# Performance work log

Hardware: AMD Instinct MI355X
Metric: run time of the kernel (lower is better)

## Reference

```python
import jax, jax.numpy as jnp
import numpy as np

B, S, E, H = 2, 2048, 768, 12
DK = E // H


def setup_inputs() -> dict:
    key = jax.random.key(0)
    ks = jax.random.split(key, 8)
    scale = 1.0 / np.sqrt(E)
    return {
        "key": jax.random.normal(ks[0], (B, S, E), jnp.float32),
        "query": jax.random.normal(ks[1], (B, S, E), jnp.float32),
        "value": jax.random.normal(ks[2], (B, S, E), jnp.float32),
        "mask": jax.random.randint(ks[3], (1, 1, S, S), 0, 2, jnp.int32),
        # nn.Linear params (w_k used for q/k/v as in the source; w_o output proj)
        "Wk": jax.random.uniform(ks[4], (E, E), jnp.float32, -scale, scale),
        "bk": jax.random.uniform(ks[5], (E,), jnp.float32, -scale, scale),
        "Wo": jax.random.uniform(ks[6], (E, E), jnp.float32, -scale, scale),
        "bo": jax.random.uniform(ks[7], (E,), jnp.float32, -scale, scale),
    }


def reference(key, query, value, mask, Wk, bk, Wo, bo):
    # NOTE: source module (faithfully) projects q, k, v all with w_k.
    k = (key @ Wk.T + bk).reshape(B, S, H, DK).transpose(0, 2, 1, 3)    # [B,H,S,DK]
    q = (query @ Wk.T + bk).reshape(B, S, H, DK).transpose(0, 2, 1, 3)
    v = (value @ Wk.T + bk).reshape(B, S, H, DK).transpose(0, 2, 1, 3)
    # quirk: scores MULTIPLIED by sqrt(d_k) (source bug, preserved)
    scores = jnp.einsum("bhsd,bhtd->bhst", q, k) * jnp.sqrt(jnp.float32(DK))
    # quirk: masked positions set to 1e-6 (not -inf), BEFORE softmax
    scores = jnp.where(mask == 0, jnp.float32(1e-6), scores)
    # dropout=0.0 -> identity (applied pre-softmax in source)
    attn = jax.nn.softmax(scores, axis=-1)                               # [B,H,S,S]
    x = jnp.einsum("bhst,bhtd->bhsd", attn, v)                           # [B,H,S,DK]
    x = x.transpose(0, 2, 1, 3).reshape(B, S, E)
    return x @ Wo.T + bo
```

## Files before the change

### kernel.cpp

```cpp
#include <hip/hip_runtime.h>

#define BB 2
#define SS 2048
#define EE 768
#define HH 12
#define DKK 64

typedef _Float16 h16;
typedef _Float16 half8 __attribute__((ext_vector_type(8)));
typedef _Float16 h16x4 __attribute__((ext_vector_type(4)));
typedef float f32x4 __attribute__((ext_vector_type(4)));

__global__ void pack_mask_k(const int* __restrict__ mask, unsigned* __restrict__ mp) {
    int idx = blockIdx.x * 256 + threadIdx.x;
    int base = idx * 32;
    const int4* m4 = (const int4*)(mask + base);
    unsigned w = 0;
#pragma unroll
    for (int i = 0; i < 8; ++i) {
        int4 v = m4[i];
        if (v.x) w |= 1u << (i * 4 + 0);
        if (v.y) w |= 1u << (i * 4 + 1);
        if (v.z) w |= 1u << (i * 4 + 2);
        if (v.w) w |= 1u << (i * 4 + 3);
    }
    mp[idx] = w;
}

__launch_bounds__(256)
__global__ void proj_gemm_k(const float* __restrict__ srcK, const float* __restrict__ srcQ,
                            const float* __restrict__ srcV, const float* __restrict__ Wk,
                            const float* __restrict__ bk,
                            h16* __restrict__ kh, h16* __restrict__ qh, h16* __restrict__ vtp) {
    __shared__ h16 As[128 * 64];
    __shared__ h16 Bs[128 * 64];
    const int bid = blockIdx.x;
    const int idx = (bid & 7) * 72 + (bid >> 3);
    const int z = idx / 192;
    const int rem = idx % 192;
    const int n0 = (rem % 6) * 128, m0 = (rem / 6) * 128;
    const float* src = (z == 0) ? srcK : ((z == 1) ? srcQ : srcV);
    const int tid = threadIdx.x, lane = tid & 63, wid = tid >> 6;
    const int wr = wid >> 1, wc = wid & 1;
    f32x4 acc[4][4] = {};

    for (int k0 = 0; k0 < EE; k0 += 64) {
#pragma unroll
        for (int it = 0; it < 4; ++it) {
            int e8 = it * 256 + tid;
            int row = e8 >> 3, g = e8 & 7;
            const float* pa = src + (m0 + row) * EE + k0 + g * 8;
            const float* pb = Wk + (n0 + row) * EE + k0 + g * 8;
            float4 a0 = *(const float4*)pa, a1 = *(const float4*)(pa + 4);
            float4 b0 = *(const float4*)pb, b1 = *(const float4*)(pb + 4);
            half8 ha = {(h16)a0.x, (h16)a0.y, (h16)a0.z, (h16)a0.w,
                        (h16)a1.x, (h16)a1.y, (h16)a1.z, (h16)a1.w};
            half8 hb = {(h16)b0.x, (h16)b0.y, (h16)b0.z, (h16)b0.w,
                        (h16)b1.x, (h16)b1.y, (h16)b1.z, (h16)b1.w};
            int sw = (g ^ (row & 7)) << 4;
            *(half8*)((char*)As + row * 128 + sw) = ha;
            *(half8*)((char*)Bs + row * 128 + sw) = hb;
        }
        __syncthreads();
#pragma unroll
        for (int ks = 0; ks < 2; ++ks) {
            half8 a[4], b[4];
#pragma unroll
            for (int rf = 0; rf < 4; ++rf) {
                int row = wr * 64 + rf * 16 + (lane & 15);
                int g = (ks * 4 + (lane >> 4)) ^ (row & 7);
                a[rf] = *(const half8*)((const char*)As + row * 128 + (g << 4));
            }
#pragma unroll
            for (int cf = 0; cf < 4; ++cf) {
                int row = wc * 64 + cf * 16 + (lane & 15);
                int g = (ks * 4 + (lane >> 4)) ^ (row & 7);
                b[cf] = *(const half8*)((const char*)Bs + row * 128 + (g << 4));
            }
#pragma unroll
            for (int rf = 0; rf < 4; ++rf)
#pragma unroll
                for (int cf = 0; cf < 4; ++cf)
                    acc[rf][cf] = __builtin_amdgcn_mfma_f32_16x16x32_f16(a[rf], b[cf], acc[rf][cf], 0, 0, 0);
        }
        __syncthreads();
    }
    if (z == 2) {
#pragma unroll
        for (int rf = 0; rf < 4; ++rf)
#pragma unroll
            for (int cf = 0; cf < 4; ++cf) {
                int n = n0 + wc * 64 + cf * 16 + (lane & 15);
                float bias = bk[n];
                int h = n >> 6, d = n & 63;
                int mb = m0 + wr * 64 + rf * 16 + (lane >> 4) * 4;
                int b = mb >> 11, s = mb & 2047;
                h16x4 pv = {(h16)(acc[rf][cf][0] + bias), (h16)(acc[rf][cf][1] + bias),
                            (h16)(acc[rf][cf][2] + bias), (h16)(acc[rf][cf][3] + bias)};
                *(h16x4*)(vtp + ((long)((b * HH + h) * 64 + d)) * SS + s) = pv;
            }
    } else {
        h16* dst = (z == 0) ? kh : qh;
#pragma unroll
        for (int rf = 0; rf < 4; ++rf)
#pragma unroll
            for (int cf = 0; cf < 4; ++cf) {
                int n = n0 + wc * 64 + cf * 16 + (lane & 15);
                float bias = bk[n];
                int h = n >> 6, d = n & 63;
#pragma unroll
                for (int j = 0; j < 4; ++j) {
                    int m = m0 + wr * 64 + rf * 16 + (lane >> 4) * 4 + j;
                    int b = m >> 11, s = m & 2047;
                    dst[(((long)(b * HH + h) * SS + s) << 6) + d] = (h16)(acc[rf][cf][j] + bias);
                }
            }
    }
}

struct StageRegs { half8 k[2], v[2]; };

__device__ __forceinline__ void ld_stage(StageRegs& r, const h16* __restrict__ kg,
                                         const h16* __restrict__ vg,
                                         int kv0, int wid, int lane) {
    int rr = lane >> 3;
    int sg = (lane & 7) ^ rr;
#pragma unroll
    for (int i = 0; i < 2; ++i) {
        int row = wid * 16 + i * 8 + rr;
        r.k[i] = *(const half8*)(kg + (long)(kv0 + row) * DKK + sg * 8);
        r.v[i] = *(const half8*)(vg + (long)row * SS + kv0 + sg * 8);
    }
}

__device__ __forceinline__ void st_stage(h16* __restrict__ kl, h16* __restrict__ vl,
                                         const StageRegs& r, int wid, int lane) {
#pragma unroll
    for (int i = 0; i < 2; ++i) {
        *(half8*)(kl + wid * 1024 + i * 512 + lane * 8) = r.k[i];
        *(half8*)(vl + wid * 1024 + i * 512 + lane * 8) = r.v[i];
    }
}

__launch_bounds__(256, 3)
__global__ void attn_k(const h16* __restrict__ qh, const h16* __restrict__ kh,
                       const h16* __restrict__ vt, const unsigned long long* __restrict__ mp,
                       h16* __restrict__ xh) {
    __shared__ h16 Kbuf[2][4096];
    __shared__ h16 Vbuf[2][4096];
    __shared__ char Ps[8192];
    const int tid = threadIdx.x;
    const int lane = tid & 63, wid = tid >> 6;
    const int l = lane & 15, g = lane >> 4;
    const int bid = blockIdx.x;
    const int idx = (bid & 7) * 96 + (bid >> 3);
    const int q0 = (idx & 31) * 64 + wid * 16;
    const int bh = idx >> 5;
    const long base = (long)bh * SS * DKK;
    const h16* kg = kh + base;
    const h16* vg = vt + base;
    char* pbase = Ps + wid * 2048;

    half8 qf0, qf1;
    {
        const h16* qp = qh + base + (long)(q0 + l) * DKK + g * 8;
        qf0 = *(const half8*)qp;
        qf1 = *(const half8*)(qp + 32);
    }
    const unsigned long long* mrow = mp + (long)(q0 + l) * (SS / 64);

    f32x4 o[4] = {};
    float m2 = -INFINITY, lsum = 0.f;
    const float K2 = 8.0f * 1.44269504f;
    const float C2 = 1e-6f * 1.44269504f;

    StageRegs sr;
    ld_stage(sr, kg, vg, 0, wid, lane);
    st_stage(Kbuf[0], Vbuf[0], sr, wid, lane);
    __syncthreads();

    for (int t = 0; t < 32; ++t) {
        const h16* Kl = Kbuf[t & 1];
        const h16* Vl = Vbuf[t & 1];
        ld_stage(sr, kg, vg, ((t + 1) & 31) * 64, wid, lane);
        half8 ka[4], kb[4];
#pragma unroll
        for (int cf = 0; cf < 4; ++cf) {
            int row = cf * 16 + l;
            const h16* kp = Kl + row * 64;
            ka[cf] = *(const half8*)(kp + ((g ^ (row & 7)) << 3));
            kb[cf] = *(const half8*)(kp + (((4 + g) ^ (row & 7)) << 3));
        }
        f32x4 s[4];
        __builtin_amdgcn_s_setprio(1);
#pragma unroll
        for (int cf = 0; cf < 4; ++cf) {
            f32x4 z = {};
            z = __builtin_amdgcn_mfma_f32_16x16x32_f16(ka[cf], qf0, z, 0, 0, 0);
            z = __builtin_amdgcn_mfma_f32_16x16x32_f16(kb[cf], qf1, z, 0, 0, 0);
            s[cf] = z;
        }
        __builtin_amdgcn_s_setprio(0);
        unsigned long long mw = mrow[t];
        unsigned w0 = (unsigned)mw, w1 = (unsigned)(mw >> 32);
#pragma unroll
        for (int cf = 0; cf < 4; ++cf) {
            unsigned wcb = (cf & 2) ? w1 : w0;
#pragma unroll
            for (int j = 0; j < 4; ++j) {
                unsigned sh = ((cf & 1) << 4) + g * 4 + j;
                s[cf][j] = ((wcb >> sh) & 1u) ? s[cf][j] * K2 : C2;
            }
        }
        float pmax = fmaxf(fmaxf(s[0][0], s[0][1]), fmaxf(s[0][2], s[0][3]));
#pragma unroll
        for (int cf = 1; cf < 4; ++cf)
            pmax = fmaxf(pmax, fmaxf(fmaxf(s[cf][0], s[cf][1]), fmaxf(s[cf][2], s[cf][3])));
        if (!__all(pmax <= m2 + 11.0f)) {
            pmax = fmaxf(pmax, __shfl_xor(pmax, 16));
            pmax = fmaxf(pmax, __shfl_xor(pmax, 32));
            float mnew = fmaxf(m2, pmax);
            float alpha = __builtin_amdgcn_exp2f(m2 - mnew);
#pragma unroll
            for (int df = 0; df < 4; ++df)
#pragma unroll
                for (int j = 0; j < 4; ++j) o[df][j] *= alpha;
            lsum *= alpha;
            m2 = mnew;
        }
        float rs = 0.f;
#pragma unroll
        for (int cf = 0; cf < 4; ++cf)
#pragma unroll
            for (int j = 0; j < 4; ++j) {
                float p = __builtin_amdgcn_exp2f(s[cf][j] - m2);
                s[cf][j] = p;
                rs += p;
            }
        lsum += rs;
#pragma unroll
        for (int cf = 0; cf < 4; ++cf) {
            h16x4 pk = {(h16)s[cf][0], (h16)s[cf][1], (h16)s[cf][2], (h16)s[cf][3]};
            int gran = (2 * cf + (g >> 1)) ^ (l & 7);
            *(h16x4*)(pbase + l * 128 + gran * 16 + (g & 1) * 8) = pk;
        }
#pragma unroll
        for (int ks = 0; ks < 2; ++ks) {
            int gr = (ks * 4 + g) ^ (l & 7);
            half8 pf = *(const half8*)(pbase + l * 128 + gr * 16);
            half8 vk[4];
#pragma unroll
            for (int df = 0; df < 4; ++df) {
                int row = df * 16 + l;
                vk[df] = *(const half8*)(Vl + row * 64 + (((ks * 4 + g) ^ (row & 7)) << 3));
            }
            __builtin_amdgcn_s_setprio(1);
#pragma unroll
            for (int df = 0; df < 4; ++df)
                o[df] = __builtin_amdgcn_mfma_f32_16x16x32_f16(vk[df], pf, o[df], 0, 0, 0);
            __builtin_amdgcn_s_setprio(0);
        }
        st_stage(Kbuf[(t + 1) & 1], Vbuf[(t + 1) & 1], sr, wid, lane);
        __syncthreads();
    }

    lsum += __shfl_xor(lsum, 16);
    lsum += __shfl_xor(lsum, 32);
    float inv = 1.0f / lsum;
    int b = bh / HH, h = bh % HH;
    h16* xp = xh + (long)(b * SS + q0 + l) * EE + h * 64 + g * 4;
#pragma unroll
    for (int df = 0; df < 4; ++df) {
        h16x4 v4 = {(h16)(o[df][0] * inv), (h16)(o[df][1] * inv),
                    (h16)(o[df][2] * inv), (h16)(o[df][3] * inv)};
        *(h16x4*)(xp + df * 16) = v4;
    }
}

__launch_bounds__(256)
__global__ void out_gemm_k(const h16* __restrict__ xh, const float* __restrict__ Wo,
                           const float* __restrict__ bo, float* __restrict__ out) {
    __shared__ h16 As[128 * 64];
    __shared__ h16 Bs[128 * 64];
    const int bid = blockIdx.x;
    const int idx = (bid & 7) * 24 + (bid >> 3);
    const int n0 = (idx % 6) * 128, m0 = (idx / 6) * 128;
    const int tid = threadIdx.x, lane = tid & 63, wid = tid >> 6;
    const int wr = wid >> 1, wc = wid & 1;
    f32x4 acc[4][4] = {};

    for (int k0 = 0; k0 < EE; k0 += 64) {
#pragma unroll
        for (int it = 0; it < 4; ++it) {
            int e8 = it * 256 + tid;
            int row = e8 >> 3, g = e8 & 7;
            half8 ha = *(const half8*)(xh + (m0 + row) * EE + k0 + g * 8);
            const float* pb = Wo + (n0 + row) * EE + k0 + g * 8;
            float4 b0 = *(const float4*)pb, b1 = *(const float4*)(pb + 4);
            half8 hb = {(h16)b0.x, (h16)b0.y, (h16)b0.z, (h16)b0.w,
                        (h16)b1.x, (h16)b1.y, (h16)b1.z, (h16)b1.w};
            int sw = (g ^ (row & 7)) << 4;
            *(half8*)((char*)As + row * 128 + sw) = ha;
            *(half8*)((char*)Bs + row * 128 + sw) = hb;
        }
        __syncthreads();
#pragma unroll
        for (int ks = 0; ks < 2; ++ks) {
            half8 a[4], b[4];
#pragma unroll
            for (int rf = 0; rf < 4; ++rf) {
                int row = wr * 64 + rf * 16 + (lane & 15);
                int g = (ks * 4 + (lane >> 4)) ^ (row & 7);
                a[rf] = *(const half8*)((const char*)As + row * 128 + (g << 4));
            }
#pragma unroll
            for (int cf = 0; cf < 4; ++cf) {
                int row = wc * 64 + cf * 16 + (lane & 15);
                int g = (ks * 4 + (lane >> 4)) ^ (row & 7);
                b[cf] = *(const half8*)((const char*)Bs + row * 128 + (g << 4));
            }
#pragma unroll
            for (int rf = 0; rf < 4; ++rf)
#pragma unroll
                for (int cf = 0; cf < 4; ++cf)
                    acc[rf][cf] = __builtin_amdgcn_mfma_f32_16x16x32_f16(a[rf], b[cf], acc[rf][cf], 0, 0, 0);
        }
        __syncthreads();
    }
#pragma unroll
    for (int rf = 0; rf < 4; ++rf)
#pragma unroll
        for (int cf = 0; cf < 4; ++cf) {
            int n = n0 + wc * 64 + cf * 16 + (lane & 15);
            float bias = bo[n];
#pragma unroll
            for (int j = 0; j < 4; ++j) {
                int m = m0 + wr * 64 + rf * 16 + (lane >> 4) * 4 + j;
                out[(long)m * EE + n] = acc[rf][cf][j] + bias;
            }
        }
}

extern "C" void kernel_launch(void* const* d_in, const int* in_sizes, int n_in,
                              void* d_out, int out_size, void* d_ws, size_t ws_size,
                              hipStream_t stream) {
    const float* key   = (const float*)d_in[0];
    const float* query = (const float*)d_in[1];
    const float* value = (const float*)d_in[2];
    const int*   mask  = (const int*)d_in[3];
    const float* Wk    = (const float*)d_in[4];
    const float* bk    = (const float*)d_in[5];
    const float* Wo    = (const float*)d_in[6];
    const float* bo    = (const float*)d_in[7];

    char* ws = (char*)d_ws;
    h16* qh = (h16*)(ws + 0);
    h16* kh = (h16*)(ws + 6291456);
    h16* vt = (h16*)(ws + 12582912);
    h16* xh = (h16*)(ws + 18874368);
    unsigned* mp = (unsigned*)(ws + 25165824);
    float* out = (float*)d_out;

    hipLaunchKernelGGL(pack_mask_k, dim3(SS * SS / 32 / 256), dim3(256), 0, stream, mask, mp);
    hipLaunchKernelGGL(proj_gemm_k, dim3(576), dim3(256), 0, stream,
                       key, query, value, Wk, bk, kh, qh, vt);
    hipLaunchKernelGGL(attn_k, dim3(SS / 64 * BB * HH), dim3(256), 0, stream,
                       qh, kh, vt, (const unsigned long long*)mp, xh);
    hipLaunchKernelGGL(out_gemm_k, dim3(192), dim3(256), 0, stream, xh, Wo, bo, out);
}
```

Baseline: 132.0 us.

## Prefetch next K-tile into registers in projection and output GEMMs

Both the QKV projection GEMM and the output GEMM now load the next 64-wide K-slice from global memory into registers before running the MFMAs on the current shared-memory tile. The prefetched data is converted and written to LDS after the compute, so global load latency overlaps with matrix math. MFMA sections are also wrapped in s_setprio to raise wave priority. This adds register pressure from the staged float4 buffers, which could reduce occupancy.

```diff
diff --git a/kernel.cpp b/kernel.cpp
--- a/kernel.cpp
+++ b/kernel.cpp
@@ -44,24 +44,39 @@
     const int wr = wid >> 1, wc = wid & 1;
     f32x4 acc[4][4] = {};
 
+    float4 ra[4][2], rb[4][2];
+#define PROJ_ISSUE(k0)                                                        \
+    _Pragma("unroll")                                                         \
+    for (int it = 0; it < 4; ++it) {                                          \
+        int e8 = it * 256 + tid;                                              \
+        int row = e8 >> 3, g = e8 & 7;                                        \
+        const float* pa = src + (m0 + row) * EE + (k0) + g * 8;               \
+        const float* pb = Wk + (n0 + row) * EE + (k0) + g * 8;                \
+        ra[it][0] = *(const float4*)pa; ra[it][1] = *(const float4*)(pa + 4); \
+        rb[it][0] = *(const float4*)pb; rb[it][1] = *(const float4*)(pb + 4); \
+    }
+#define PROJ_WRITE()                                                          \
+    _Pragma("unroll")                                                         \
+    for (int it = 0; it < 4; ++it) {                                          \
+        int e8 = it * 256 + tid;                                              \
+        int row = e8 >> 3, g = e8 & 7;                                        \
+        half8 ha = {(h16)ra[it][0].x, (h16)ra[it][0].y, (h16)ra[it][0].z,     \
+                    (h16)ra[it][0].w, (h16)ra[it][1].x, (h16)ra[it][1].y,     \
+                    (h16)ra[it][1].z, (h16)ra[it][1].w};                      \
+        half8 hb = {(h16)rb[it][0].x, (h16)rb[it][0].y, (h16)rb[it][0].z,     \
+                    (h16)rb[it][0].w, (h16)rb[it][1].x, (h16)rb[it][1].y,     \
+                    (h16)rb[it][1].z, (h16)rb[it][1].w};                      \
+        int sw = (g ^ (row & 7)) << 4;                                        \
+        *(half8*)((char*)As + row * 128 + sw) = ha;                           \
+        *(half8*)((char*)Bs + row * 128 + sw) = hb;                           \
+    }
+
+    PROJ_ISSUE(0)
+    PROJ_WRITE()
+    __syncthreads();
+
     for (int k0 = 0; k0 < EE; k0 += 64) {
-#pragma unroll
-        for (int it = 0; it < 4; ++it) {
-            int e8 = it * 256 + tid;
-            int row = e8 >> 3, g = e8 & 7;
-            const float* pa = src + (m0 + row) * EE + k0 + g * 8;
-            const float* pb = Wk + (n0 + row) * EE + k0 + g * 8;
-            float4 a0 = *(const float4*)pa, a1 = *(const float4*)(pa + 4);
-            float4 b0 = *(const float4*)pb, b1 = *(const float4*)(pb + 4);
-            half8 ha = {(h16)a0.x, (h16)a0.y, (h16)a0.z, (h16)a0.w,
-                        (h16)a1.x, (h16)a1.y, (h16)a1.z, (h16)a1.w};
-            half8 hb = {(h16)b0.x, (h16)b0.y, (h16)b0.z, (h16)b0.w,
-                        (h16)b1.x, (h16)b1.y, (h16)b1.z, (h16)b1.w};
-            int sw = (g ^ (row & 7)) << 4;
-            *(half8*)((char*)As + row * 128 + sw) = ha;
-            *(half8*)((char*)Bs + row * 128 + sw) = hb;
-        }
-        __syncthreads();
+        if (k0 + 64 < EE) { PROJ_ISSUE(k0 + 64) }
 #pragma unroll
         for (int ks = 0; ks < 2; ++ks) {
             half8 a[4], b[4];
@@ -77,14 +92,22 @@
                 int g = (ks * 4 + (lane >> 4)) ^ (row & 7);
                 b[cf] = *(const half8*)((const char*)Bs + row * 128 + (g << 4));
             }
+            __builtin_amdgcn_s_setprio(1);
 #pragma unroll
             for (int rf = 0; rf < 4; ++rf)
 #pragma unroll
                 for (int cf = 0; cf < 4; ++cf)
                     acc[rf][cf] = __builtin_amdgcn_mfma_f32_16x16x32_f16(a[rf], b[cf], acc[rf][cf], 0, 0, 0);
+            __builtin_amdgcn_s_setprio(0);
         }
         __syncthreads();
-    }
+        if (k0 + 64 < EE) {
+            PROJ_WRITE()
+            __syncthreads();
+        }
+    }
+#undef PROJ_ISSUE
+#undef PROJ_WRITE
     if (z == 2) {
 #pragma unroll
         for (int rf = 0; rf < 4; ++rf)
@@ -289,21 +312,36 @@
     const int wr = wid >> 1, wc = wid & 1;
     f32x4 acc[4][4] = {};
 
+    half8 ra[4];
+    float4 rb[4][2];
+#define OG_ISSUE(k0)                                                          \
+    _Pragma("unroll")                                                         \
+    for (int it = 0; it < 4; ++it) {                                          \
+        int e8 = it * 256 + tid;                                              \
+        int row = e8 >> 3, g = e8 & 7;                                        \
+        ra[it] = *(const half8*)(xh + (m0 + row) * EE + (k0) + g * 8);        \
+        const float* pb = Wo + (n0 + row) * EE + (k0) + g * 8;                \
+        rb[it][0] = *(const float4*)pb; rb[it][1] = *(const float4*)(pb + 4); \
+    }
+#define OG_WRITE()                                                            \
+    _Pragma("unroll")                                                         \
+    for (int it = 0; it < 4; ++it) {                                          \
+        int e8 = it * 256 + tid;                                              \
+        int row = e8 >> 3, g = e8 & 7;                                        \
+        half8 hb = {(h16)rb[it][0].x, (h16)rb[it][0].y, (h16)rb[it][0].z,     \
+                    (h16)rb[it][0].w, (h16)rb[it][1].x, (h16)rb[it][1].y,     \
+                    (h16)rb[it][1].z, (h16)rb[it][1].w};                      \
+        int sw = (g ^ (row & 7)) << 4;                                        \
+        *(half8*)((char*)As + row * 128 + sw) = ra[it];                       \
+        *(half8*)((char*)Bs + row * 128 + sw) = hb;                           \
+    }
+
+    OG_ISSUE(0)
+    OG_WRITE()
+    __syncthreads();
+
     for (int k0 = 0; k0 < EE; k0 += 64) {
-#pragma unroll
-        for (int it = 0; it < 4; ++it) {
-            int e8 = it * 256 + tid;
-            int row = e8 >> 3, g = e8 & 7;
-            half8 ha = *(const half8*)(xh + (m0 + row) * EE + k0 + g * 8);
-            const float* pb = Wo + (n0 + row) * EE + k0 + g * 8;
-            float4 b0 = *(const float4*)pb, b1 = *(const float4*)(pb + 4);
-            half8 hb = {(h16)b0.x, (h16)b0.y, (h16)b0.z, (h16)b0.w,
-                        (h16)b1.x, (h16)b1.y, (h16)b1.z, (h16)b1.w};
-            int sw = (g ^ (row & 7)) << 4;
-            *(half8*)((char*)As + row * 128 + sw) = ha;
-            *(half8*)((char*)Bs + row * 128 + sw) = hb;
-        }
-        __syncthreads();
+        if (k0 + 64 < EE) { OG_ISSUE(k0 + 64) }
 #pragma unroll
         for (int ks = 0; ks < 2; ++ks) {
             half8 a[4], b[4];
@@ -319,14 +357,22 @@
                 int g = (ks * 4 + (lane >> 4)) ^ (row & 7);
                 b[cf] = *(const half8*)((const char*)Bs + row * 128 + (g << 4));
             }
+            __builtin_amdgcn_s_setprio(1);
 #pragma unroll
             for (int rf = 0; rf < 4; ++rf)
 #pragma unroll
                 for (int cf = 0; cf < 4; ++cf)
                     acc[rf][cf] = __builtin_amdgcn_mfma_f32_16x16x32_f16(a[rf], b[cf], acc[rf][cf], 0, 0, 0);
+            __builtin_amdgcn_s_setprio(0);
         }
         __syncthreads();
-    }
+        if (k0 + 64 < EE) {
+            OG_WRITE()
+            __syncthreads();
+        }
+    }
+#undef OG_ISSUE
+#undef OG_WRITE
 #pragma unroll
     for (int rf = 0; rf < 4; ++rf)
 #pragma unroll
```

Result: slower. 138.5 us (+5.0%).
